# Optimization experiments

Hardware: AMD Instinct MI355X
Metric: run time of the kernel (lower is better)

## Reference

```python
import jax, jax.numpy as jnp
import numpy as np

B, T, N = 256, 512, 128
GO, EOS = 1, 2  # mead-baseline Offsets
NEG = -10000.0


def setup_inputs() -> dict:
    key = jax.random.key(0)
    k1, k2, k3 = jax.random.split(key, 3)
    unaries = jax.random.normal(k1, (B, T, N), dtype=jnp.float32)
    # constraint mask: True where transition is INVALID (masked to -1e4)
    cmask = jax.random.bernoulli(k2, 0.3, (1, N, N))
    trans = jax.nn.log_softmax(
        jnp.where(cmask, jnp.float32(NEG), jnp.float32(0.0)), axis=1
    )  # [1, N, N], matches buffer construction in __init__
    lengths = jax.random.randint(k3, (B,), T // 2, T + 1).astype(jnp.int64)
    lengths = lengths.at[0].set(T)  # ensure max(lengths) == T
    return {"unaries": unaries, "trans": trans, "lengths": lengths}


def _viterbi(probv, trans, lengths, start_idx, end_idx):
    # probv: [T, B, N] log-probs; trans: [1, N, N]; lengths: [B]
    seq_len, batch, n_tags = probv.shape
    trans0 = trans[0]  # [N(cur), N(prev)]
    lengths = lengths.astype(jnp.int32)

    alphas = jnp.full((batch, n_tags), NEG, probv.dtype).at[:, start_idx].set(0.0)
    alphas = jax.nn.log_softmax(alphas, axis=-1)

    def step(alphas, xs):
        unary_t, i = xs  # [B, N], scalar
        ntv = alphas[:, None, :] + trans0[None]          # [B, N_cur, N_prev]
        bp = jnp.argmax(ntv, axis=2)                     # backpointers [B, N]
        new_alphas = jnp.max(ntv, axis=2) + unary_t      # [B, N]
        alphas = jnp.where((i < lengths)[:, None], new_alphas, alphas)
        return alphas, bp

    alphas, bps = jax.lax.scan(step, alphas, (probv, jnp.arange(seq_len)))

    terminal = alphas + trans0[end_idx][None, :]         # [B, N]
    path_score = jnp.max(terminal, axis=1)               # [B]
    best_tag = jnp.argmax(terminal, axis=1)              # [B]

    rev_len = seq_len - lengths - 1

    def back(btid, xs):
        bp, i = xs  # bp: [B, N]
        new = jnp.take_along_axis(bp, btid[:, None], axis=1)[:, 0]
        btid = jnp.where(i > rev_len, new, btid)
        return btid, btid

    _, ys = jax.lax.scan(back, best_tag, (bps[::-1], jnp.arange(seq_len)))
    full = jnp.concatenate([best_tag[None], ys], axis=0)  # [T+1, B]
    best_path = full[:seq_len][::-1]                       # [T, B]

    seq_mask = jnp.arange(seq_len)[:, None] < lengths[None, :]  # [T, B]
    best_path = jnp.where(seq_mask, best_path, 0)
    return best_path, path_score


def reference(unaries, trans, lengths):
    # constrained branch of TaggerGreedyDecoder.forward (batch_first=True)
    probv = jax.nn.log_softmax(jnp.swapaxes(unaries, 0, 1), axis=-1)  # [T,B,N]
    preds_tb, scores = _viterbi(probv, trans, lengths, GO, EOS)
    return jnp.swapaxes(preds_tb, 0, 1), scores  # ([B,T], [B])
```

## Files before the change

kernel.cpp:

```cpp
#include <hip/hip_runtime.h>

#define BB 256
#define TT 512
#define NN 128
#define GO_IDX 1
#define EOS_IDX 2
#define TSPLIT 496
#define NEGV (-10000.0f)
#define ASLOT(x) ((x) + (((x) >> 5) << 2))

__global__ __launch_bounds__(256) void lsm_kernel(float* __restrict__ u) {
    const int wave = threadIdx.x >> 6, lane = threadIdx.x & 63;
    const int gw = blockIdx.x * 4 + wave;
    const int NW = 2048 * 4;
    const int R  = BB * TT;
    float2* base = (float2*)u;
    int row = gw;
    float2 v = base[(size_t)row * 64 + lane];
    while (row < R) {
        const int nrow = row + NW;
        float2 vn = make_float2(0.f, 0.f);
        if (nrow < R) vn = base[(size_t)nrow * 64 + lane];
        float m = fmaxf(v.x, v.y);
#pragma unroll
        for (int off = 32; off; off >>= 1) m = fmaxf(m, __shfl_xor(m, off, 64));
        float s = expf(v.x - m) + expf(v.y - m);
#pragma unroll
        for (int off = 32; off; off >>= 1) s += __shfl_xor(s, off, 64);
        float ls = logf(s);
        base[(size_t)row * 64 + lane] = make_float2((v.x - m) - ls, (v.y - m) - ls);
        v = vn; row = nrow;
    }
}

__global__ __launch_bounds__(512) void viterbi_kernel(
    const float* __restrict__ probs,
    const float* __restrict__ trans,
    const int*   __restrict__ lengths_raw,
    float* __restrict__ out,
    unsigned char* __restrict__ ws)
{
    __shared__ unsigned char bps[(TSPLIT - 1) * NN];
    __shared__ __align__(16) float alpha[2][144];
    __shared__ float fin_v[2];
    __shared__ int   fin_i[2];

    const int tid  = threadIdx.x;
    const int b    = blockIdx.x;
    const int wave = tid >> 6;
    const int lane = tid & 63;
    const int q    = tid & 3;
    const int cur  = tid >> 2;

    int len;
    {
        int probe = lengths_raw[1];
        len = (probe == 0) ? lengths_raw[2 * b] : lengths_raw[b];
    }

    float tr[32];
    {
        const float4* t4 = (const float4*)(trans + cur * NN + q * 32);
#pragma unroll
        for (int i = 0; i < 8; ++i) {
            float4 v = t4[i];
            tr[4*i+0] = v.x; tr[4*i+1] = v.y; tr[4*i+2] = v.z; tr[4*i+3] = v.w;
        }
    }

    if (tid < NN) alpha[0][ASLOT(tid)] = (tid == GO_IDX) ? 0.0f : NEGV;

    const float* pb = probs + (size_t)b * TT * NN;
    unsigned char* wst = ws + (size_t)b * ((TT - TSPLIT) * NN);

    float P[8], Nx[8];
    if (q == 0) {
#pragma unroll
        for (int k = 0; k < 8; ++k) P[k] = pb[k * NN + cur];
    }
    __syncthreads();

    const int nG = (len + 7) >> 3;
    for (int g = 0; g < nG; ++g) {
        const int tb = g * 8;
        if (q == 0) {
#pragma unroll
            for (int k = 0; k < 8; ++k) {
                int tt = tb + 8 + k; if (tt > TT - 1) tt = TT - 1;
                Nx[k] = pb[tt * NN + cur];
            }
        }
#pragma unroll
        for (int k = 0; k < 8; ++k) {
            const int t = tb + k;
            if (t < len) {
                const float* ra = alpha[t & 1];
                float*       wa = alpha[(t & 1) ^ 1];
                const float4* a4 = (const float4*)(ra + q * 36);
                float bv[4]; int bi[4];
#pragma unroll
                for (int c = 0; c < 4; ++c) {
                    bv[c] = -INFINITY; bi[c] = 0;
#pragma unroll
                    for (int r = 0; r < 2; ++r) {
                        float4 a = a4[c * 2 + r];
                        const int base = c * 8 + r * 4;
                        float x0 = a.x + tr[base + 0]; if (x0 > bv[c]) { bv[c] = x0; bi[c] = base + 0; }
                        float x1 = a.y + tr[base + 1]; if (x1 > bv[c]) { bv[c] = x1; bi[c] = base + 1; }
                        float x2 = a.z + tr[base + 2]; if (x2 > bv[c]) { bv[c] = x2; bi[c] = base + 2; }
                        float x3 = a.w + tr[base + 3]; if (x3 > bv[c]) { bv[c] = x3; bi[c] = base + 3; }
                    }
                }
                float best = bv[0]; int bp = bi[0];
#pragma unroll
                for (int c = 1; c < 4; ++c) { if (bv[c] > best) { best = bv[c]; bp = bi[c]; } }
                bp += q * 32;

                float v1 = __shfl_xor(best, 1, 64);
                float m1 = fmaxf(best, v1);
                float v2 = __shfl_xor(m1, 2, 64);
                float M  = fmaxf(m1, v2);
                bool iw = ((q & 1) ? (best > v1) : (best >= v1)) &&
                          ((q & 2) ? (m1 > v2)   : (m1 >= v2));
                if (t >= 1 && iw) {
                    if (t < TSPLIT) bps[(t - 1) * NN + cur] = (unsigned char)bp;
                    else            wst[(t - TSPLIT) * NN + cur] = (unsigned char)bp;
                }
                if (q == 0) wa[ASLOT(cur)] = M + P[k];
                __syncthreads();
            }
        }
#pragma unroll
        for (int k = 0; k < 8; ++k) P[k] = Nx[k];
    }

    __threadfence();

    if (tid < NN) {
        float v = alpha[len & 1][ASLOT(tid)] + trans[EOS_IDX * NN + tid];
        int idx = tid;
#pragma unroll
        for (int off = 32; off; off >>= 1) {
            float ov = __shfl_xor(v, off, 64);
            int   oi = __shfl_xor(idx, off, 64);
            if (ov > v || (ov == v && oi < idx)) { v = ov; idx = oi; }
        }
        if (lane == 0) { fin_v[wave] = v; fin_i[wave] = idx; }
    }
    __syncthreads();

    for (int t = len + tid; t < TT; t += 512) out[(size_t)b * TT + t] = 0.0f;

    if (tid == 0) {
        float v0 = fin_v[0], v1 = fin_v[1];
        int   i0 = fin_i[0], i1 = fin_i[1];
        float sc; int tag;
        if (v1 > v0) { sc = v1; tag = i1; }
        else         { sc = v0; tag = i0; }
        out[(size_t)BB * TT + b] = sc;

        for (int t = len - 1; t >= 0; --t) {
            out[(size_t)b * TT + t] = (float)tag;
            if (t >= 1) {
                int nb;
                if (t < TSPLIT) nb = bps[(t - 1) * NN + tag];
                else            nb = ((volatile const unsigned char*)wst)[(t - TSPLIT) * NN + tag];
                tag = nb;
            }
        }
    }
}

extern "C" void kernel_launch(void* const* d_in, const int* in_sizes, int n_in,
                              void* d_out, int out_size, void* d_ws, size_t ws_size,
                              hipStream_t stream) {
    float*       unaries = (float*)d_in[0];
    const float* trans   = (const float*)d_in[1];
    const int*   lengths = (const int*)d_in[2];
    float* out = (float*)d_out;
    unsigned char* ws = (unsigned char*)d_ws;

    hipLaunchKernelGGL(lsm_kernel, dim3(2048), dim3(256), 0, stream, unaries);
    hipLaunchKernelGGL(viterbi_kernel, dim3(BB), dim3(512), 0, stream,
                       unaries, trans, lengths, out, ws);
}
```

Before: 568.2 us.

## Split each Viterbi state over 8 threads and vectorize log-softmax rows

The Viterbi kernel now uses 1024 threads per block, with 8 threads per current tag instead of 4. Each thread scans 16 previous tags rather than 32, and a third shuffle stage completes the argmax. This shortens the serial per-timestep chain at the cost of more threads waiting at every __syncthreads and a longer reduction. The log-softmax kernel now handles each row with 32 lanes using float4 loads, in a fixed 8-iteration unrolled loop with prefetch.

```diff
diff --git a/kernel.cpp b/kernel.cpp
--- a/kernel.cpp
+++ b/kernel.cpp
@@ -7,33 +7,34 @@
 #define EOS_IDX 2
 #define TSPLIT 496
 #define NEGV (-10000.0f)
-#define ASLOT(x) ((x) + (((x) >> 5) << 2))
+#define ASLOT(x) ((x) + (((x) >> 4) << 2))
 
 __global__ __launch_bounds__(256) void lsm_kernel(float* __restrict__ u) {
-    const int wave = threadIdx.x >> 6, lane = threadIdx.x & 63;
-    const int gw = blockIdx.x * 4 + wave;
-    const int NW = 2048 * 4;
-    const int R  = BB * TT;
-    float2* base = (float2*)u;
-    int row = gw;
-    float2 v = base[(size_t)row * 64 + lane];
-    while (row < R) {
-        const int nrow = row + NW;
-        float2 vn = make_float2(0.f, 0.f);
-        if (nrow < R) vn = base[(size_t)nrow * 64 + lane];
-        float m = fmaxf(v.x, v.y);
+    const int g0 = (blockIdx.x * 256 + threadIdx.x) >> 5;
+    const int l  = threadIdx.x & 31;
+    const int NG = 2048 * 8;
+    float4* base = (float4*)u;
+    int row = g0;
+    float4 v = base[(size_t)row * 32 + l];
 #pragma unroll
-        for (int off = 32; off; off >>= 1) m = fmaxf(m, __shfl_xor(m, off, 64));
-        float s = expf(v.x - m) + expf(v.y - m);
+    for (int it = 0; it < 8; ++it) {
+        const int nrow = row + NG;
+        float4 vn = make_float4(0.f, 0.f, 0.f, 0.f);
+        if (it < 7) vn = base[(size_t)nrow * 32 + l];
+        float m = fmaxf(fmaxf(v.x, v.y), fmaxf(v.z, v.w));
 #pragma unroll
-        for (int off = 32; off; off >>= 1) s += __shfl_xor(s, off, 64);
+        for (int off = 16; off; off >>= 1) m = fmaxf(m, __shfl_xor(m, off, 64));
+        float s = expf(v.x - m) + expf(v.y - m) + expf(v.z - m) + expf(v.w - m);
+#pragma unroll
+        for (int off = 16; off; off >>= 1) s += __shfl_xor(s, off, 64);
         float ls = logf(s);
-        base[(size_t)row * 64 + lane] = make_float2((v.x - m) - ls, (v.y - m) - ls);
+        base[(size_t)row * 32 + l] =
+            make_float4((v.x - m) - ls, (v.y - m) - ls, (v.z - m) - ls, (v.w - m) - ls);
         v = vn; row = nrow;
     }
 }
 
-__global__ __launch_bounds__(512) void viterbi_kernel(
+__global__ __launch_bounds__(1024) void viterbi_kernel(
     const float* __restrict__ probs,
     const float* __restrict__ trans,
     const int*   __restrict__ lengths_raw,
@@ -41,7 +42,7 @@
     unsigned char* __restrict__ ws)
 {
     __shared__ unsigned char bps[(TSPLIT - 1) * NN];
-    __shared__ __align__(16) float alpha[2][144];
+    __shared__ __align__(16) float alpha[2][160];
     __shared__ float fin_v[2];
     __shared__ int   fin_i[2];
 
@@ -49,8 +50,8 @@
     const int b    = blockIdx.x;
     const int wave = tid >> 6;
     const int lane = tid & 63;
-    const int q    = tid & 3;
-    const int cur  = tid >> 2;
+    const int q    = tid & 7;
+    const int cur  = tid >> 3;
 
     int len;
     {
@@ -58,11 +59,11 @@
         len = (probe == 0) ? lengths_raw[2 * b] : lengths_raw[b];
     }
 
-    float tr[32];
+    float tr[16];
     {
-        const float4* t4 = (const float4*)(trans + cur * NN + q * 32);
+        const float4* t4 = (const float4*)(trans + cur * NN + q * 16);
 #pragma unroll
-        for (int i = 0; i < 8; ++i) {
+        for (int i = 0; i < 4; ++i) {
             float4 v = t4[i];
             tr[4*i+0] = v.x; tr[4*i+1] = v.y; tr[4*i+2] = v.z; tr[4*i+3] = v.w;
         }
@@ -96,33 +97,32 @@
             if (t < len) {
                 const float* ra = alpha[t & 1];
                 float*       wa = alpha[(t & 1) ^ 1];
-                const float4* a4 = (const float4*)(ra + q * 36);
+                const float4* a4 = (const float4*)(ra + q * 20);
                 float bv[4]; int bi[4];
 #pragma unroll
                 for (int c = 0; c < 4; ++c) {
-                    bv[c] = -INFINITY; bi[c] = 0;
-#pragma unroll
-                    for (int r = 0; r < 2; ++r) {
-                        float4 a = a4[c * 2 + r];
-                        const int base = c * 8 + r * 4;
-                        float x0 = a.x + tr[base + 0]; if (x0 > bv[c]) { bv[c] = x0; bi[c] = base + 0; }
-                        float x1 = a.y + tr[base + 1]; if (x1 > bv[c]) { bv[c] = x1; bi[c] = base + 1; }
-                        float x2 = a.z + tr[base + 2]; if (x2 > bv[c]) { bv[c] = x2; bi[c] = base + 2; }
-                        float x3 = a.w + tr[base + 3]; if (x3 > bv[c]) { bv[c] = x3; bi[c] = base + 3; }
-                    }
+                    float4 a = a4[c];
+                    const int base = c * 4;
+                    bv[c] = a.x + tr[base + 0]; bi[c] = base + 0;
+                    float x1 = a.y + tr[base + 1]; if (x1 > bv[c]) { bv[c] = x1; bi[c] = base + 1; }
+                    float x2 = a.z + tr[base + 2]; if (x2 > bv[c]) { bv[c] = x2; bi[c] = base + 2; }
+                    float x3 = a.w + tr[base + 3]; if (x3 > bv[c]) { bv[c] = x3; bi[c] = base + 3; }
                 }
                 float best = bv[0]; int bp = bi[0];
 #pragma unroll
                 for (int c = 1; c < 4; ++c) { if (bv[c] > best) { best = bv[c]; bp = bi[c]; } }
-                bp += q * 32;
+                bp += q * 16;
 
                 float v1 = __shfl_xor(best, 1, 64);
+                bool  w1 = (q & 1) ? (best > v1) : (best >= v1);
                 float m1 = fmaxf(best, v1);
                 float v2 = __shfl_xor(m1, 2, 64);
-                float M  = fmaxf(m1, v2);
-                bool iw = ((q & 1) ? (best > v1) : (best >= v1)) &&
-                          ((q & 2) ? (m1 > v2)   : (m1 >= v2));
-                if (t >= 1 && iw) {
+                bool  w2 = (q & 2) ? (m1 > v2) : (m1 >= v2);
+                float m2 = fmaxf(m1, v2);
+                float v4 = __shfl_xor(m2, 4, 64);
+                bool  w3 = (q & 4) ? (m2 > v4) : (m2 >= v4);
+                float M  = fmaxf(m2, v4);
+                if (t >= 1 && (w1 && w2 && w3)) {
                     if (t < TSPLIT) bps[(t - 1) * NN + cur] = (unsigned char)bp;
                     else            wst[(t - TSPLIT) * NN + cur] = (unsigned char)bp;
                 }
@@ -147,9 +147,9 @@
         }
         if (lane == 0) { fin_v[wave] = v; fin_i[wave] = idx; }
     }
+
+    for (int t = len + tid; t < TT; t += 1024) out[(size_t)b * TT + t] = 0.0f;
     __syncthreads();
-
-    for (int t = len + tid; t < TT; t += 512) out[(size_t)b * TT + t] = 0.0f;
 
     if (tid == 0) {
         float v0 = fin_v[0], v1 = fin_v[1];
@@ -181,6 +181,6 @@
     unsigned char* ws = (unsigned char*)d_ws;
 
     hipLaunchKernelGGL(lsm_kernel, dim3(2048), dim3(256), 0, stream, unaries);
-    hipLaunchKernelGGL(viterbi_kernel, dim3(BB), dim3(512), 0, stream,
+    hipLaunchKernelGGL(viterbi_kernel, dim3(BB), dim3(1024), 0, stream,
                        unaries, trans, lengths, out, ws);
 }
```

New measurement: 589.7 us. +3.8%, slower.
